# Performance work log

Hardware: AMD Instinct MI355X
Metric: run time of the kernel (lower is better)

Reference implementation:

```python
import jax, jax.numpy as jnp
import numpy as np

N_NODES = 100000

def _gcn_norm(edge_index, num_nodes):
    # PyG GCNConv: add self-loops, symmetric normalization deg^-1/2 A_hat deg^-1/2
    loop = jnp.arange(num_nodes, dtype=edge_index.dtype)
    src = jnp.concatenate([edge_index[0], loop])  # [E+N]
    dst = jnp.concatenate([edge_index[1], loop])  # [E+N]
    deg = jax.ops.segment_sum(jnp.ones(dst.shape[0], jnp.float32), dst, num_segments=num_nodes)
    dis = jnp.where(deg > 0, jax.lax.rsqrt(deg), 0.0)
    norm = dis[src] * dis[dst]  # [E+N]
    return src, dst, norm

def _gcn_layer(x, W, b, src, dst, norm, num_nodes):
    xw = x @ W                                   # [N, H] dense GEMM first (out_dim <= in_dim)
    msg = xw[src] * norm[:, None]                # gather + scale per edge
    out = jax.ops.segment_sum(msg, dst, num_segments=num_nodes)  # scatter-add
    return out + b

def setup_inputs() -> dict:
    key = jax.random.key(0)
    ks = jax.random.split(key, 6)
    E = 1600000
    return {
        "x": jax.random.normal(ks[0], (N_NODES, 512), jnp.float32),
        "edge_index": jax.random.randint(ks[1], (2, E), 0, N_NODES, dtype=jnp.int64),
        "W1": jax.random.normal(ks[2], (512, 256), jnp.float32) * 0.04,
        "b1": jnp.zeros((256,), jnp.float32),
        "W2": jax.random.normal(ks[3], (256, 256), jnp.float32) * 0.06,
        "b2": jnp.zeros((256,), jnp.float32),
        "fc_w": jax.random.normal(ks[4], (256, 128), jnp.float32) * 0.06,
        "fc_b": jnp.zeros((128,), jnp.float32),
    }

def reference(x, edge_index, W1, b1, W2, b2, fc_w, fc_b):
    src, dst, norm = _gcn_norm(edge_index, N_NODES)
    h = jax.nn.relu(_gcn_layer(x, W1, b1, src, dst, norm, N_NODES))
    h = jax.nn.relu(_gcn_layer(h, W2, b2, src, dst, norm, N_NODES))
    return h @ fc_w + fc_b
```

## Files before the change

### kernel.cpp

```cpp
#include <hip/hip_runtime.h>


#define N_NODES 100000
constexpr int D_IN  = 512;
constexpr int D_H   = 256;
constexpr int D_OUT = 128;
constexpr int M_PAD = 100096;

typedef _Float16 f16x8 __attribute__((ext_vector_type(8)));
typedef _Float16 f16x4 __attribute__((ext_vector_type(4)));
typedef float f32x4 __attribute__((ext_vector_type(4)));

#define GLD16(SRC, DST) __builtin_amdgcn_global_load_lds(                      \
    (const __attribute__((address_space(1))) void*)(SRC),                      \
    (__attribute__((address_space(3))) void*)(DST), 16, 0, 0)

__global__ __launch_bounds__(256) void zero_deg_k(int* __restrict__ deg) {
  int i = (blockIdx.x * 256 + threadIdx.x) * 4;
  if (i < N_NODES) *(int4*)(deg + i) = make_int4(0, 0, 0, 0);
}

__global__ __launch_bounds__(256) void wtrans_k(const float* __restrict__ W1,
                                                const float* __restrict__ W2,
                                                const float* __restrict__ FC,
                                                _Float16* __restrict__ w1t,
                                                _Float16* __restrict__ w2t,
                                                _Float16* __restrict__ fct) {
  int i = blockIdx.x * 256 + threadIdx.x;
  if (i < 131072) {
    int k = i >> 8, n = i & 255;
    w1t[(size_t)n * 512 + k] = (_Float16)W1[i];
  } else if (i < 196608) {
    int j = i - 131072;
    int k = j >> 8, n = j & 255;
    w2t[(size_t)n * 256 + k] = (_Float16)W2[j];
  } else if (i < 229376) {
    int j = i - 196608;
    int k = j >> 7, n = j & 127;
    fct[(size_t)n * 256 + k] = (_Float16)FC[j];
  }
}

__global__ __launch_bounds__(256) void deg_count_k(const int* __restrict__ dst,
                                                   int* __restrict__ deg,
                                                   int* __restrict__ pe, int E) {
  int i = (blockIdx.x * 256 + threadIdx.x) * 4;
  if (i + 3 < E) {
    int4 d = *(const int4*)(dst + i);
    int4 p;
    p.x = atomicAdd(&deg[d.x], 1);
    p.y = atomicAdd(&deg[d.y], 1);
    p.z = atomicAdd(&deg[d.z], 1);
    p.w = atomicAdd(&deg[d.w], 1);
    *(int4*)(pe + i) = p;
  } else {
    for (int t = i; t < E; ++t) pe[t] = atomicAdd(&deg[dst[t]], 1);
  }
}

__global__ __launch_bounds__(256) void scan1_k(const int* __restrict__ deg,
                                               int* __restrict__ off,
                                               int* __restrict__ bsum,
                                               float* __restrict__ dis, int n) {
  __shared__ int ts[256];
  const int tid = threadIdx.x;
  const int base = blockIdx.x * 1024 + tid * 4;
  int v[4];
#pragma unroll
  for (int t = 0; t < 4; ++t) v[t] = (base + t < n) ? deg[base + t] : 0;
#pragma unroll
  for (int t = 0; t < 4; ++t)
    if (base + t < n) dis[base + t] = rsqrtf((float)v[t] + 1.0f);
  const int tot = v[0] + v[1] + v[2] + v[3];
  ts[tid] = tot;
  __syncthreads();
  for (int o = 1; o < 256; o <<= 1) {
    int t = (tid >= o) ? ts[tid - o] : 0;
    __syncthreads();
    ts[tid] += t;
    __syncthreads();
  }
  int run = ts[tid] - tot;
#pragma unroll
  for (int t = 0; t < 4; ++t) {
    if (base + t < n) off[base + t] = run;
    run += v[t];
  }
  if (tid == 255) bsum[blockIdx.x] = ts[255];
}

__global__ __launch_bounds__(128) void scan2_k(int* __restrict__ bsum, int nb) {
  __shared__ int ts[128];
  const int tid = threadIdx.x;
  const int v = (tid < nb) ? bsum[tid] : 0;
  ts[tid] = v;
  __syncthreads();
  for (int o = 1; o < 128; o <<= 1) {
    int t = (tid >= o) ? ts[tid - o] : 0;
    __syncthreads();
    ts[tid] += t;
    __syncthreads();
  }
  if (tid < nb) bsum[tid] = ts[tid] - v;
}

__global__ __launch_bounds__(256) void fill_k(const int* __restrict__ src,
                                              const int* __restrict__ dst,
                                              const int* __restrict__ pe,
                                              const int* __restrict__ off,
                                              const int* __restrict__ bsum,
                                              int* __restrict__ ssorted, int E) {
  int i = (blockIdx.x * 256 + threadIdx.x) * 4;
  if (i + 3 < E) {
    int4 s = *(const int4*)(src + i);
    int4 d = *(const int4*)(dst + i);
    int4 p = *(const int4*)(pe + i);
    ssorted[off[d.x] + bsum[d.x >> 10] + p.x] = s.x;
    ssorted[off[d.y] + bsum[d.y >> 10] + p.y] = s.y;
    ssorted[off[d.z] + bsum[d.z >> 10] + p.z] = s.z;
    ssorted[off[d.w] + bsum[d.w >> 10] + p.w] = s.w;
  } else {
    for (int t = i; t < E; ++t) {
      int d = dst[t];
      ssorted[off[d] + bsum[d >> 10] + pe[t]] = src[t];
    }
  }
}

template<int BN, bool AF32, bool OUT_Y>
__global__ __launch_bounds__(512, 4) void gemm_glds_k(
    const float* __restrict__ Af32,
    const _Float16* __restrict__ A16,
    const _Float16* __restrict__ Bt,
    const float* __restrict__ bias,
    const float* __restrict__ dis,
    float* __restrict__ C,
    _Float16* __restrict__ Y,
    int M, int K) {
  constexpr int BM = 128, BK = 32;
  constexpr int FN   = BN / 64;
  constexpr int NBI  = BN / 128;
  constexpr int ASZ  = BM * BK;
  constexpr int AFSZ = BM * BK;
  constexpr int BSZ  = BN * BK;
  constexpr int EPAD = 4;
  constexpr int SMEM_F16 = AF32 ? 2 * (2 * AFSZ + BSZ) : 3 * (ASZ + BSZ);

  __shared__ __align__(16) _Float16 smem[SMEM_F16];
  float* epi = (float*)smem;

  const int tid  = threadIdx.x;
  const int w    = tid >> 6, lane = tid & 63;
  const int wm   = w >> 2, wn = w & 3;
  const int l15  = lane & 15, l16 = lane >> 4;
  const int row0 = blockIdx.y * BM;

  f32x4 acc[4][FN];
#pragma unroll
  for (int i = 0; i < 4; ++i)
#pragma unroll
    for (int j = 0; j < FN; ++j) acc[i][j] = (f32x4){0.f, 0.f, 0.f, 0.f};

  const int nsteps = K >> 5;

  const int lr = lane >> 2, lg = lane & 3;
  const int brow0 = w * (NBI * 16) + lr;
  const int brow1 = brow0 + 16;
  const _Float16* srcB0 = Bt + (size_t)brow0 * K + ((lg ^ (brow0 & 3)) << 3);
  const _Float16* srcB1 = Bt + (size_t)brow1 * K + ((lg ^ (brow1 & 3)) << 3);

  if constexpr (AF32) {
    float* Asf = (float*)smem;
    _Float16* Bs = smem + 4 * AFSZ;
    const int lr8 = lane >> 3, lg8 = lane & 7;
    const int ar0 = w * 16 + lr8, ar1 = ar0 + 8;
    int g0 = row0 + ar0; if (g0 >= M) g0 = M - 1;
    int g1 = row0 + ar1; if (g1 >= M) g1 = M - 1;
    const float* srcA0 = Af32 + (size_t)g0 * K + ((lg8 ^ (lr8 & 7)) << 2);
    const float* srcA1 = Af32 + (size_t)g1 * K + ((lg8 ^ (lr8 & 7)) << 2);
    float*    dA0 = Asf + (w * 16) * BK;
    float*    dA1 = dA0 + 8 * BK;
    _Float16* dB0 = &Bs[(w * (NBI * 16)) * BK];
    _Float16* dB1 = &Bs[(w * (NBI * 16) + 16) * BK];

    auto stage = [&](int t) {
      const int kt = t << 5;
      const int pa = (t & 1) * AFSZ, pb = (t & 1) * BSZ;
      GLD16(srcA0 + kt, dA0 + pa);
      GLD16(srcA1 + kt, dA1 + pa);
      GLD16(srcB0 + kt, dB0 + pb);
      if constexpr (NBI == 2) GLD16(srcB1 + kt, dB1 + pb);
    };

    stage(0);
    __syncthreads();
    for (int t = 0; t < nsteps; ++t) {
      if (t + 1 < nsteps) stage(t + 1);
      const float* as = Asf + (t & 1) * AFSZ;
      const _Float16* bs = Bs + (t & 1) * BSZ;
      f16x8 a[4], b[FN];
#pragma unroll
      for (int i = 0; i < 4; ++i) {
        const int r = wm * 64 + i * 16 + l15;
        const float* ar = as + r * BK;
        const int s = r & 7;
        float4 lo = *(const float4*)(ar + (((2 * l16) ^ s) << 2));
        float4 hi = *(const float4*)(ar + (((2 * l16 + 1) ^ s) << 2));
        a[i][0] = (_Float16)lo.x; a[i][1] = (_Float16)lo.y;
        a[i][2] = (_Float16)lo.z; a[i][3] = (_Float16)lo.w;
        a[i][4] = (_Float16)hi.x; a[i][5] = (_Float16)hi.y;
        a[i][6] = (_Float16)hi.z; a[i][7] = (_Float16)hi.w;
      }
#pragma unroll
      for (int j = 0; j < FN; ++j) {
        const int n = wn * (FN * 16) + j * 16 + l15;
        b[j] = *(const f16x8*)&bs[n * BK + ((l16 ^ (n & 3)) << 3)];
      }
#pragma unroll
      for (int i = 0; i < 4; ++i)
#pragma unroll
        for (int j = 0; j < FN; ++j)
          acc[i][j] = __builtin_amdgcn_mfma_f32_16x16x32_f16(a[i], b[j], acc[i][j], 0, 0, 0);
      __syncthreads();
    }
  } else {
    _Float16* As = smem;
    _Float16* Bs = smem + 3 * ASZ;
    const int arow = w * 16 + lr;
    const _Float16* srcA = A16 + (size_t)(row0 + arow) * K + ((lg ^ (arow & 3)) << 3);
    _Float16* dstA  = &As[(w * 16) * BK];
    _Float16* dstB0 = &Bs[(w * (NBI * 16)) * BK];
    _Float16* dstB1 = &Bs[(w * (NBI * 16) + 16) * BK];

    auto stage = [&](int t, int buf) {
      const int kt = t << 5;
      GLD16(srcA + kt, dstA + buf * ASZ);
      GLD16(srcB0 + kt, dstB0 + buf * BSZ);
      if constexpr (NBI == 2) GLD16(srcB1 + kt, dstB1 + buf * BSZ);
    };

    stage(0, 0);
    if (nsteps > 1) stage(1, 1);

    int rbuf = 0, wbuf = 2;
    for (int t = 0; t < nsteps; ++t) {
      if (t + 1 < nsteps) {
        if constexpr (NBI == 2) asm volatile("s_waitcnt vmcnt(3)" ::: "memory");
        else                    asm volatile("s_waitcnt vmcnt(2)" ::: "memory");
      } else {
        asm volatile("s_waitcnt vmcnt(0)" ::: "memory");
      }
      __builtin_amdgcn_sched_barrier(0);
      __builtin_amdgcn_s_barrier();
      __builtin_amdgcn_sched_barrier(0);

      if (t + 2 < nsteps) stage(t + 2, wbuf);

      const _Float16* as = As + rbuf * ASZ;
      const _Float16* bs = Bs + rbuf * BSZ;
      f16x8 a[4], b[FN];
#pragma unroll
      for (int i = 0; i < 4; ++i) {
        const int r = wm * 64 + i * 16 + l15;
        a[i] = *(const f16x8*)&as[r * BK + ((l16 ^ (r & 3)) << 3)];
      }
#pragma unroll
      for (int j = 0; j < FN; ++j) {
        const int n = wn * (FN * 16) + j * 16 + l15;
        b[j] = *(const f16x8*)&bs[n * BK + ((l16 ^ (n & 3)) << 3)];
      }
#pragma unroll
      for (int i = 0; i < 4; ++i)
#pragma unroll
        for (int j = 0; j < FN; ++j)
          acc[i][j] = __builtin_amdgcn_mfma_f32_16x16x32_f16(a[i], b[j], acc[i][j], 0, 0, 0);

      rbuf = (rbuf == 2) ? 0 : rbuf + 1;
      wbuf = (wbuf == 2) ? 0 : wbuf + 1;
    }
    __syncthreads();
  }

  constexpr int ESTR = BN + EPAD;
  constexpr int CPT  = BN / 16;
#pragma unroll
  for (int c = 0; c < 4; ++c) {
    if (wm == (c >> 1)) {
      const int ib = (c & 1) * 2;
#pragma unroll
      for (int ii = 0; ii < 2; ++ii) {
        const int i = ib + ii;
#pragma unroll
        for (int j = 0; j < FN; ++j) {
          const int col = wn * (FN * 16) + j * 16 + l15;
#pragma unroll
          for (int r = 0; r < 4; ++r) {
            const int lrow = ii * 16 + l16 * 4 + r;
            epi[lrow * ESTR + col] = acc[i][j][r];
          }
        }
      }
    }
    __syncthreads();
    {
      const int lrow = tid >> 4;
      const int grow = row0 + c * 32 + lrow;
      const int colb = (tid & 15) * CPT;
      if (grow < M) {
        float v[CPT];
#pragma unroll
        for (int q = 0; q < CPT; q += 4)
          *(float4*)&v[q] = *(const float4*)&epi[lrow * ESTR + colb + q];
        if constexpr (OUT_Y) {
          const float dv = dis[grow];
          f16x8 o[CPT / 8];
#pragma unroll
          for (int q = 0; q < CPT; ++q) o[q >> 3][q & 7] = (_Float16)(v[q] * dv);
#pragma unroll
          for (int q = 0; q < CPT / 8; ++q)
            *(f16x8*)(Y + (size_t)grow * BN + colb + q * 8) = o[q];
        } else {
#pragma unroll
          for (int q = 0; q < CPT; ++q) v[q] += bias[colb + q];
#pragma unroll
          for (int q = 0; q < CPT; q += 4)
            *(float4*)(C + (size_t)grow * BN + colb + q) = *(const float4*)&v[q];
        }
      }
    }
    __syncthreads();
  }
}

__global__ __launch_bounds__(256) void gather_k(const _Float16* __restrict__ y,
                                                const int* __restrict__ ssorted,
                                                const int* __restrict__ off,
                                                const int* __restrict__ bsum,
                                                const float* __restrict__ dis,
                                                const float* __restrict__ bias,
                                                _Float16* __restrict__ h,
                                                int n, int E) {
  const int gid = blockIdx.x * 256 + threadIdx.x;
  const int v = gid >> 6, lane = gid & 63;
  if (v >= n) return;

  const float dv = dis[v];
  const int fo = lane * 4;

  f16x4 sv = *(const f16x4*)(y + (size_t)v * 256 + fo);
  float4 acc = make_float4((float)sv[0], (float)sv[1], (float)sv[2], (float)sv[3]);

  const int beg = off[v] + bsum[v >> 10];
  const int end = (v + 1 < n) ? (off[v + 1] + bsum[(v + 1) >> 10]) : E;
  const int ne = end - beg;

  for (int j0 = 0; j0 < ne; j0 += 64) {
    const int rem = ne - j0;
    const int cnt = rem < 64 ? rem : 64;
    int s_l = 0;
    if (lane < cnt) s_l = ssorted[beg + j0 + lane];

    int k = 0;
    for (; k + 8 <= cnt; k += 8) {
      f16x4 yv[8];
#pragma unroll
      for (int u = 0; u < 8; ++u) {
        const int s = __shfl(s_l, k + u);
        yv[u] = *(const f16x4*)(y + (size_t)s * 256 + fo);
      }
#pragma unroll
      for (int u = 0; u < 8; ++u) {
        acc.x += (float)yv[u][0];
        acc.y += (float)yv[u][1];
        acc.z += (float)yv[u][2];
        acc.w += (float)yv[u][3];
      }
    }
    for (; k < cnt; ++k) {
      const int s = __shfl(s_l, k);
      const f16x4 yv = *(const f16x4*)(y + (size_t)s * 256 + fo);
      acc.x += (float)yv[0];
      acc.y += (float)yv[1];
      acc.z += (float)yv[2];
      acc.w += (float)yv[3];
    }
  }

  const float4 b = *(const float4*)(bias + fo);
  f16x4 o;
  o[0] = (_Float16)fmaxf(fmaf(dv, acc.x, b.x), 0.f);
  o[1] = (_Float16)fmaxf(fmaf(dv, acc.y, b.y), 0.f);
  o[2] = (_Float16)fmaxf(fmaf(dv, acc.z, b.z), 0.f);
  o[3] = (_Float16)fmaxf(fmaf(dv, acc.w, b.w), 0.f);
  *(f16x4*)(h + (size_t)v * 256 + fo) = o;
}

extern "C" void kernel_launch(void* const* d_in, const int* in_sizes, int n_in,
                              void* d_out, int out_size, void* d_ws, size_t ws_size,
                              hipStream_t stream) {
  const float* x    = (const float*)d_in[0];
  const int*   ei   = (const int*)d_in[1];
  const float* W1   = (const float*)d_in[2];
  const float* b1   = (const float*)d_in[3];
  const float* W2   = (const float*)d_in[4];
  const float* b2   = (const float*)d_in[5];
  const float* fc_w = (const float*)d_in[6];
  const float* fc_b = (const float*)d_in[7];
  float* out = (float*)d_out;

  const int E = in_sizes[1] / 2;
  const int* src = ei;
  const int* dst = ei + E;
  const int N = N_NODES;

  char* p = (char*)d_ws;
  int*   deg     = (int*)p;            p += (size_t)N * 4;
  float* dis     = (float*)p;          p += (size_t)N * 4;
  int*   off     = (int*)p;            p += (size_t)(N + 1) * 4;
  int*   pe      = (int*)p;            p += (size_t)E * 4;
  int*   ssorted = (int*)p;            p += (size_t)E * 4;
  int*   bsum    = (int*)p;            p += 512;
  p = (char*)(((size_t)p + 255) & ~(size_t)255);
  _Float16* w1t = (_Float16*)p;        p += (size_t)D_H   * D_IN * 2;
  _Float16* w2t = (_Float16*)p;        p += (size_t)D_H   * D_H  * 2;
  _Float16* fct = (_Float16*)p;        p += (size_t)D_OUT * D_H  * 2;
  p = (char*)(((size_t)p + 255) & ~(size_t)255);
  _Float16* y16 = (_Float16*)p;        p += (size_t)M_PAD * D_H * 2;
  _Float16* h16 = (_Float16*)p;        p += (size_t)M_PAD * D_H * 2;

  wtrans_k<<<896, 256, 0, stream>>>(W1, W2, fc_w, w1t, w2t, fct);
  zero_deg_k<<<(N / 4 + 255) / 256, 256, 0, stream>>>(deg);

  const int NB1 = (N + 1023) / 1024;
  const int EB4 = ((E + 3) / 4 + 255) / 256;
  deg_count_k<<<EB4, 256, 0, stream>>>(dst, deg, pe, E);
  scan1_k<<<NB1, 256, 0, stream>>>(deg, off, bsum, dis, N);
  scan2_k<<<1, 128, 0, stream>>>(bsum, NB1);
  fill_k<<<EB4, 256, 0, stream>>>(src, dst, pe, off, bsum, ssorted, E);

  const int node_wave_blocks = (N * 64 + 255) / 256;
  const dim3 gg(1, M_PAD / 128);

  gemm_glds_k<256, true, true><<<gg, 512, 0, stream>>>(
      x, nullptr, w1t, nullptr, dis, nullptr, y16, N, D_IN);
  gather_k<<<node_wave_blocks, 256, 0, stream>>>(y16, ssorted, off, bsum, dis, b1, h16, N, E);

  gemm_glds_k<256, false, true><<<gg, 512, 0, stream>>>(
      nullptr, h16, w2t, nullptr, dis, nullptr, y16, N, D_H);
  gather_k<<<node_wave_blocks, 256, 0, stream>>>(y16, ssorted, off, bsum, dis, b2, h16, N, E);

  gemm_glds_k<128, false, false><<<gg, 512, 0, stream>>>(
      nullptr, h16, fct, fc_b, nullptr, out, nullptr, N, D_H);
}
```

Measured before the change: 482.2 us.

## Fuse final aggregation with FC GEMM and merge small prep/scan kernels

Adds a kernel that aggregates the second GCN layer for 16 nodes per block into shared memory and immediately applies the final FC layer with MFMA. This avoids writing h16 to memory and reading it back for a separate GEMM. Zeroing of the degree array is folded into the weight-transpose kernel. The two scan kernels are merged using a last-block ticket pattern. Together these cut three launches and one full activation round-trip, at the cost of fewer waves per node in the gather (4 nodes per wave processed serially) and reduced GEMM tile efficiency.

```diff
diff --git a/kernel.cpp b/kernel.cpp
--- a/kernel.cpp
+++ b/kernel.cpp
@@ -15,18 +15,17 @@
     (const __attribute__((address_space(1))) void*)(SRC),                      \
     (__attribute__((address_space(3))) void*)(DST), 16, 0, 0)
 
-__global__ __launch_bounds__(256) void zero_deg_k(int* __restrict__ deg) {
-  int i = (blockIdx.x * 256 + threadIdx.x) * 4;
-  if (i < N_NODES) *(int4*)(deg + i) = make_int4(0, 0, 0, 0);
-}
-
-__global__ __launch_bounds__(256) void wtrans_k(const float* __restrict__ W1,
-                                                const float* __restrict__ W2,
-                                                const float* __restrict__ FC,
-                                                _Float16* __restrict__ w1t,
-                                                _Float16* __restrict__ w2t,
-                                                _Float16* __restrict__ fct) {
+__global__ __launch_bounds__(256) void prep_k(const float* __restrict__ W1,
+                                              const float* __restrict__ W2,
+                                              const float* __restrict__ FC,
+                                              _Float16* __restrict__ w1t,
+                                              _Float16* __restrict__ w2t,
+                                              _Float16* __restrict__ fct,
+                                              int* __restrict__ deg,
+                                              int* __restrict__ ticket) {
   int i = blockIdx.x * 256 + threadIdx.x;
+  if (i == 0) *ticket = 0;
+  if (i * 4 < N_NODES) *(int4*)(deg + i * 4) = make_int4(0, 0, 0, 0);
   if (i < 131072) {
     int k = i >> 8, n = i & 255;
     w1t[(size_t)n * 512 + k] = (_Float16)W1[i];
@@ -58,10 +57,12 @@
   }
 }
 
-__global__ __launch_bounds__(256) void scan1_k(const int* __restrict__ deg,
-                                               int* __restrict__ off,
-                                               int* __restrict__ bsum,
-                                               float* __restrict__ dis, int n) {
+__global__ __launch_bounds__(256) void scan12_k(const int* __restrict__ deg,
+                                                int* __restrict__ off,
+                                                int* __restrict__ bsum,
+                                                float* __restrict__ dis,
+                                                int* __restrict__ ticket,
+                                                int n, int nb) {
   __shared__ int ts[256];
   const int tid = threadIdx.x;
   const int base = blockIdx.x * 1024 + tid * 4;
@@ -87,21 +88,24 @@
     run += v[t];
   }
   if (tid == 255) bsum[blockIdx.x] = ts[255];
-}
-
-__global__ __launch_bounds__(128) void scan2_k(int* __restrict__ bsum, int nb) {
-  __shared__ int ts[128];
-  const int tid = threadIdx.x;
-  const int v = (tid < nb) ? bsum[tid] : 0;
-  ts[tid] = v;
+
+  __threadfence();
+  __shared__ int amLast;
+  if (tid == 0) amLast = (atomicAdd(ticket, 1) == gridDim.x - 1) ? 1 : 0;
   __syncthreads();
-  for (int o = 1; o < 128; o <<= 1) {
-    int t = (tid >= o) ? ts[tid - o] : 0;
-    __syncthreads();
-    ts[tid] += t;
-    __syncthreads();
-  }
-  if (tid < nb) bsum[tid] = ts[tid] - v;
+  if (amLast) {
+    __threadfence();
+    int bv = (tid < nb) ? bsum[tid] : 0;
+    ts[tid] = bv;
+    __syncthreads();
+    for (int o = 1; o < 256; o <<= 1) {
+      int t = (tid >= o) ? ts[tid - o] : 0;
+      __syncthreads();
+      ts[tid] += t;
+      __syncthreads();
+    }
+    if (tid < nb) bsum[tid] = ts[tid] - bv;
+  }
 }
 
 __global__ __launch_bounds__(256) void fill_k(const int* __restrict__ src,
@@ -395,6 +399,110 @@
   *(f16x4*)(h + (size_t)v * 256 + fo) = o;
 }
 
+__global__ __launch_bounds__(256) void gather_fc_k(const _Float16* __restrict__ y,
+                                                   const int* __restrict__ ssorted,
+                                                   const int* __restrict__ off,
+                                                   const int* __restrict__ bsum,
+                                                   const float* __restrict__ dis,
+                                                   const float* __restrict__ bias,
+                                                   const _Float16* __restrict__ fct,
+                                                   const float* __restrict__ fc_b,
+                                                   float* __restrict__ out,
+                                                   int n, int E) {
+  __shared__ __align__(16) _Float16 hs[16 * 264];
+  const int tid = threadIdx.x;
+  const int w = tid >> 6, lane = tid & 63;
+  const int l15 = lane & 15, l16 = lane >> 4;
+  const int fo = lane * 4;
+
+#pragma unroll 1
+  for (int q = 0; q < 4; ++q) {
+    const int v = blockIdx.x * 16 + w * 4 + q;
+    const float dv = dis[v];
+
+    f16x4 sv = *(const f16x4*)(y + (size_t)v * 256 + fo);
+    float4 acc = make_float4((float)sv[0], (float)sv[1], (float)sv[2], (float)sv[3]);
+
+    const int beg = off[v] + bsum[v >> 10];
+    const int end = (v + 1 < n) ? (off[v + 1] + bsum[(v + 1) >> 10]) : E;
+    const int ne = end - beg;
+
+    for (int j0 = 0; j0 < ne; j0 += 64) {
+      const int rem = ne - j0;
+      const int cnt = rem < 64 ? rem : 64;
+      int s_l = 0;
+      if (lane < cnt) s_l = ssorted[beg + j0 + lane];
+      int k = 0;
+      for (; k + 8 <= cnt; k += 8) {
+        f16x4 yv[8];
+#pragma unroll
+        for (int u = 0; u < 8; ++u) {
+          const int s = __shfl(s_l, k + u);
+          yv[u] = *(const f16x4*)(y + (size_t)s * 256 + fo);
+        }
+#pragma unroll
+        for (int u = 0; u < 8; ++u) {
+          acc.x += (float)yv[u][0];
+          acc.y += (float)yv[u][1];
+          acc.z += (float)yv[u][2];
+          acc.w += (float)yv[u][3];
+        }
+      }
+      for (; k < cnt; ++k) {
+        const int s = __shfl(s_l, k);
+        const f16x4 yv = *(const f16x4*)(y + (size_t)s * 256 + fo);
+        acc.x += (float)yv[0];
+        acc.y += (float)yv[1];
+        acc.z += (float)yv[2];
+        acc.w += (float)yv[3];
+      }
+    }
+
+    const float4 b = *(const float4*)(bias + fo);
+    f16x4 o;
+    o[0] = (_Float16)fmaxf(fmaf(dv, acc.x, b.x), 0.f);
+    o[1] = (_Float16)fmaxf(fmaf(dv, acc.y, b.y), 0.f);
+    o[2] = (_Float16)fmaxf(fmaf(dv, acc.z, b.z), 0.f);
+    o[3] = (_Float16)fmaxf(fmaf(dv, acc.w, b.w), 0.f);
+    *(f16x4*)&hs[(w * 4 + q) * 264 + fo] = o;
+  }
+  __syncthreads();
+
+  f32x4 acc0 = (f32x4){0.f, 0.f, 0.f, 0.f};
+  f32x4 acc1 = (f32x4){0.f, 0.f, 0.f, 0.f};
+  const int c0 = w * 32 + l15;
+  const int c1 = c0 + 16;
+#pragma unroll
+  for (int ks = 0; ks < 8; ++ks) {
+    f16x8 a = *(const f16x8*)&hs[l15 * 264 + ks * 32 + l16 * 8];
+    f16x8 b0 = *(const f16x8*)&fct[(size_t)c0 * 256 + ks * 32 + l16 * 8];
+    f16x8 b1 = *(const f16x8*)&fct[(size_t)c1 * 256 + ks * 32 + l16 * 8];
+    acc0 = __builtin_amdgcn_mfma_f32_16x16x32_f16(a, b0, acc0, 0, 0, 0);
+    acc1 = __builtin_amdgcn_mfma_f32_16x16x32_f16(a, b1, acc1, 0, 0, 0);
+  }
+  __syncthreads();
+
+  float* os = (float*)hs;
+  {
+    const float bb0 = fc_b[c0], bb1 = fc_b[c1];
+#pragma unroll
+    for (int r = 0; r < 4; ++r) {
+      const int row = l16 * 4 + r;
+      os[row * 132 + c0] = acc0[r] + bb0;
+      os[row * 132 + c1] = acc1[r] + bb1;
+    }
+  }
+  __syncthreads();
+  {
+    const int r = tid >> 4, cb = (tid & 15) * 8;
+    float4 v0 = *(const float4*)&os[r * 132 + cb];
+    float4 v1 = *(const float4*)&os[r * 132 + cb + 4];
+    float* op = out + (size_t)(blockIdx.x * 16 + r) * 128 + cb;
+    *(float4*)op = v0;
+    *(float4*)(op + 4) = v1;
+  }
+}
+
 extern "C" void kernel_launch(void* const* d_in, const int* in_sizes, int n_in,
                               void* d_out, int out_size, void* d_ws, size_t ws_size,
                               hipStream_t stream) {
@@ -416,10 +524,11 @@
   char* p = (char*)d_ws;
   int*   deg     = (int*)p;            p += (size_t)N * 4;
   float* dis     = (float*)p;          p += (size_t)N * 4;
-  int*   off     = (int*)p;            p += (size_t)(N + 1) * 4;
+  int*   off     = (int*)p;            p += (size_t)(N + 4) * 4;
   int*   pe      = (int*)p;            p += (size_t)E * 4;
   int*   ssorted = (int*)p;            p += (size_t)E * 4;
   int*   bsum    = (int*)p;            p += 512;
+  int*   ticket  = (int*)p;            p += 256;
   p = (char*)(((size_t)p + 255) & ~(size_t)255);
   _Float16* w1t = (_Float16*)p;        p += (size_t)D_H   * D_IN * 2;
   _Float16* w2t = (_Float16*)p;        p += (size_t)D_H   * D_H  * 2;
@@ -428,14 +537,12 @@
   _Float16* y16 = (_Float16*)p;        p += (size_t)M_PAD * D_H * 2;
   _Float16* h16 = (_Float16*)p;        p += (size_t)M_PAD * D_H * 2;
 
-  wtrans_k<<<896, 256, 0, stream>>>(W1, W2, fc_w, w1t, w2t, fct);
-  zero_deg_k<<<(N / 4 + 255) / 256, 256, 0, stream>>>(deg);
+  prep_k<<<896, 256, 0, stream>>>(W1, W2, fc_w, w1t, w2t, fct, deg, ticket);
 
   const int NB1 = (N + 1023) / 1024;
   const int EB4 = ((E + 3) / 4 + 255) / 256;
   deg_count_k<<<EB4, 256, 0, stream>>>(dst, deg, pe, E);
-  scan1_k<<<NB1, 256, 0, stream>>>(deg, off, bsum, dis, N);
-  scan2_k<<<1, 128, 0, stream>>>(bsum, NB1);
+  scan12_k<<<NB1, 256, 0, stream>>>(deg, off, bsum, dis, ticket, N, NB1);
   fill_k<<<EB4, 256, 0, stream>>>(src, dst, pe, off, bsum, ssorted, E);
 
   const int node_wave_blocks = (N * 64 + 255) / 256;
@@ -447,8 +554,7 @@
 
   gemm_glds_k<256, false, true><<<gg, 512, 0, stream>>>(
       nullptr, h16, w2t, nullptr, dis, nullptr, y16, N, D_H);
-  gather_k<<<node_wave_blocks, 256, 0, stream>>>(y16, ssorted, off, bsum, dis, b2, h16, N, E);
-
-  gemm_glds_k<128, false, false><<<gg, 512, 0, stream>>>(
-      nullptr, h16, fct, fc_b, nullptr, out, nullptr, N, D_H);
-}
+
+  gather_fc_k<<<N / 16, 256, 0, stream>>>(y16, ssorted, off, bsum, dis, b2,
+                                          fct, fc_b, out, N, E);
+}
```

Result: slower. 494.2 us (+2.5%).
